# Kernel optimization log

Hardware: AMD Instinct MI355X
Metric: run time of the kernel (lower is better)

The kernel has to match this reference:

```python
import jax, jax.numpy as jnp
import numpy as np

EPS = 1e-5

def _bn(h):
    # BatchNorm1d, affine=False, track_running_stats=False -> batch stats, biased var
    m = h.mean(axis=0)
    v = h.var(axis=0)
    return (h - m) * jax.lax.rsqrt(v + EPS)

def _aggregate(x, edge_index):
    # out[i] = sum over edges (i <- j) of x[j]  + x[i] (self loop)
    dst, src = edge_index[0], edge_index[1]
    n = x.shape[0]
    return jax.ops.segment_sum(x[src], dst, num_segments=n) + x

def setup_inputs() -> dict:
    key = jax.random.key(0)
    ks = jax.random.split(key, 12)
    N, F, H, C, E = 100000, 128, 128, 40, 800000
    x = jax.random.normal(ks[0], (N, F), dtype=jnp.float32)
    edge_index = jax.random.randint(ks[1], (2, E), 0, N, dtype=jnp.int64)
    def lin(kw, kb, fan_in, fan_out):
        bound = 1.0 / np.sqrt(fan_in)
        W = jax.random.uniform(kw, (fan_in, fan_out), minval=-bound, maxval=bound, dtype=jnp.float32)
        b = jax.random.uniform(kb, (fan_out,), minval=-bound, maxval=bound, dtype=jnp.float32)
        return W, b
    W0, b0 = lin(ks[2], ks[3], F, H)
    W1, b1 = lin(ks[4], ks[5], H, H)
    W2, b2 = lin(ks[6], ks[7], H, H)
    Wl, bl = lin(ks[8], ks[9], H, C)
    return {"x": x, "edge_index": edge_index, "W0": W0, "b0": b0,
            "W1": W1, "b1": b1, "W2": W2, "b2": b2, "Wl": Wl, "bl": bl}

def reference(x, edge_index, W0, b0, W1, b1, W2, b2, Wl, bl):
    h = x
    for W, b in ((W0, b0), (W1, b1), (W2, b2)):
        h = _aggregate(h, edge_index)          # spmm(A + I, h)
        h = h @ W + b                          # Linear
        h = _bn(h)                             # BatchNorm1d (no affine)
        h = jax.nn.relu(h)
    return h @ Wl + bl
```

## Files before the change

### kernel.cpp

```cpp
#include <hip/hip_runtime.h>
#include <stdint.h>

typedef __attribute__((ext_vector_type(8))) short short8;
typedef __attribute__((ext_vector_type(4))) float floatx4;

static __device__ __forceinline__ float b2f(uint16_t b){
    return __uint_as_float(((uint32_t)b) << 16);
}
static __device__ __forceinline__ uint16_t f2b(float f){
    uint32_t u = __float_as_uint(f);
    return (uint16_t)((u + 0x7fffu + ((u >> 16) & 1u)) >> 16);
}
static __device__ __forceinline__ float blo(uint32_t v){ return __uint_as_float(v << 16); }
static __device__ __forceinline__ float bhi(uint32_t v){ return __uint_as_float(v & 0xffff0000u); }
static __device__ __forceinline__ uint32_t pack2(float a, float b){
    return ((uint32_t)f2b(b) << 16) | (uint32_t)f2b(a);
}

__global__ void k_sentinel(uint32_t* out, int nwords, uint32_t pat){
    int i = blockIdx.x * blockDim.x + threadIdx.x;
    if (i < nwords) out[i] = pat;
}

__global__ void k_zf(int* deg, int N, const uint32_t* xw, const int* ei, int* flags,
                     float* stats, int ZB){
    if ((int)blockIdx.x == ZB){
        if (threadIdx.x != 0) return;
        int odd_nz = 0;
        for (int k = 0; k < 128; k++){
            if (ei[2 * k + 1] != 0) odd_nz = 1;
        }
        flags[0] = odd_nz ? 0 : 1;
        int big = 0;
        for (int k = 0; k < 128; k++){
            float lo = __uint_as_float(xw[k] << 16);
            if (!(fabsf(lo) <= 1024.0f)) big = 1;
        }
        flags[1] = big ? 0 : 1;
        return;
    }
    if ((int)blockIdx.x == ZB + 1){
        int t = threadIdx.x;
        #pragma unroll
        for (int j = 0; j < 3; j++) stats[j * 256 + t] = 0.f;
        return;
    }
    int i = blockIdx.x * blockDim.x + threadIdx.x;
    if (i < N) deg[i] = 0;
}

__global__ void k_deg(const int* ei, int E, int* deg, uint16_t* rank, const int* flags){
    int e = blockIdx.x * blockDim.x + threadIdx.x;
    if (e < E){
        int d = flags[0] ? ei[2 * e] : ei[e];
        int r = atomicAdd(&deg[d], 1);
        rank[e] = (uint16_t)r;
    }
}

__global__ void k_scan1(const int* deg, int N, int* bsum){
    __shared__ int s[256];
    int t = threadIdx.x;
    int i = blockIdx.x * 256 + t;
    s[t] = (i < N) ? deg[i] : 0;
    __syncthreads();
    for (int off = 128; off > 0; off >>= 1){
        if (t < off) s[t] += s[t + off];
        __syncthreads();
    }
    if (t == 0) bsum[blockIdx.x] = s[0];
}

__global__ void k_scan2(int* bsum, int nb, int* rp, int N){
    __shared__ int s[512];
    int t = threadIdx.x;
    int v = (t < nb) ? bsum[t] : 0;
    s[t] = v;
    __syncthreads();
    for (int off = 1; off < 512; off <<= 1){
        int u = (t >= off) ? s[t - off] : 0;
        __syncthreads();
        s[t] += u;
        __syncthreads();
    }
    if (t < nb) bsum[t] = s[t] - v;
    if (t == 511) rp[N] = s[511];
}

__global__ void k_scan3(const int* deg, int N, const int* bpre, int* rp){
    __shared__ int s[256];
    int t = threadIdx.x;
    int i = blockIdx.x * 256 + t;
    int v = (i < N) ? deg[i] : 0;
    s[t] = v;
    __syncthreads();
    for (int off = 1; off < 256; off <<= 1){
        int u = (t >= off) ? s[t - off] : 0;
        __syncthreads();
        s[t] += u;
        __syncthreads();
    }
    if (i < N) rp[i] = bpre[blockIdx.x] + s[t] - v;
}

__global__ __launch_bounds__(256) void k_fill(const int* __restrict__ ei, int E,
                                              const int* __restrict__ rp,
                                              const uint16_t* __restrict__ rank,
                                              int* __restrict__ col,
                                              const int* __restrict__ flags, int N){
    int xcd = blockIdx.x & 7;
    int sub = blockIdx.x >> 3;
    int nsub = gridDim.x >> 3;
    int r0 = (int)(((long long)N * xcd) >> 3);
    int r1 = (int)(((long long)N * (xcd + 1)) >> 3);
    int e0 = (int)(((long long)E * sub) / nsub);
    int e1 = (int)(((long long)E * (sub + 1)) / nsub);
    int is64 = flags[0];
    for (int e = e0 + threadIdx.x; e < e1; e += 256){
        int d = is64 ? ei[2 * e] : ei[e];
        if (d >= r0 && d < r1){
            int sv = is64 ? ei[2 * (E + e)] : ei[E + e];
            int p = rp[d] + (int)rank[e];
            col[p] = sv;
        }
    }
}

__global__ void k_prep(const void* W0, const void* W1, const void* W2, const void* Wl,
                       uint16_t* Wf0, uint16_t* Wf1, uint16_t* Wf2, uint16_t* Wfl,
                       const void* b0, const void* b1, const void* b2, const void* bl,
                       float* bc, const void* x, uint16_t* hx, int NF,
                       const int* flags){
    int blk = blockIdx.x;
    int t = threadIdx.x;
    if (blk >= 218){
        if (flags[1]) return;
        int nb = gridDim.x - 218;
        int n8 = NF >> 3;
        const float4* xv = (const float4*)x;
        uint4* hv = (uint4*)hx;
        for (int i = (blk - 218) * 256 + t; i < n8; i += nb * 256){
            float4 u0 = xv[i * 2];
            float4 u1 = xv[i * 2 + 1];
            uint4 o;
            o.x = pack2(u0.x, u0.y); o.y = pack2(u0.z, u0.w);
            o.z = pack2(u1.x, u1.y); o.w = pack2(u1.z, u1.w);
            hv[i] = o;
        }
        return;
    }
    if (blk >= 216){
        int i = (blk - 216) * 256 + t;
        if (i >= 424) return;
        const void* src; int li;
        if (i < 128)      { src = b0; li = i; }
        else if (i < 256) { src = b1; li = i - 128; }
        else if (i < 384) { src = b2; li = i - 256; }
        else              { src = bl; li = i - 384; }
        bc[i] = flags[1] ? b2f(((const uint16_t*)src)[li]) : ((const float*)src)[li];
        return;
    }
    const void* W; uint16_t* Wf; int C, ntiles, lb;
    if (blk < 64)        { W = W0; Wf = Wf0; C = 128; ntiles = 8; lb = blk; }
    else if (blk < 128)  { W = W1; Wf = Wf1; C = 128; ntiles = 8; lb = blk - 64; }
    else if (blk < 192)  { W = W2; Wf = Wf2; C = 128; ntiles = 8; lb = blk - 128; }
    else                 { W = Wl; Wf = Wfl; C = 40;  ntiles = 3; lb = blk - 192; }
    int idx = lb * 256 + t;
    int total = 4 * ntiles * 512;
    if (idx >= total) return;
    int j = idx & 7;
    int lane = (idx >> 3) & 63;
    int nt = (idx >> 9) % ntiles;
    int kt = idx / (512 * ntiles);
    int k = kt * 32 + (lane >> 4) * 8 + j;
    int n = nt * 16 + (lane & 15);
    uint16_t v = 0;
    if (n < C){
        v = flags[1] ? ((const uint16_t*)W)[k * C + n]
                     : f2b(((const float*)W)[k * C + n]);
    }
    Wf[idx] = v;
}

__global__ __launch_bounds__(256) void k_ag(const uint16_t* __restrict__ Yin,
                                            const uint16_t* __restrict__ xraw,
                                            const int* __restrict__ rp,
                                            const int* __restrict__ col,
                                            uint16_t* __restrict__ Yout,
                                            const uint16_t* __restrict__ Wf,
                                            const float* __restrict__ bias,
                                            float* __restrict__ part, int N,
                                            const float* __restrict__ st,
                                            int apply_bn, float ninv,
                                            const int* __restrict__ flags){
    __shared__ __align__(16) uint16_t albs[2048];
    __shared__ float sh_sum[128], sh_ssq[128];
    int t = threadIdx.x;
    if (t < 128){ sh_sum[t] = 0.f; sh_ssq[t] = 0.f; }
    int l16 = t & 15;
    int r = t >> 4;
    int row = blockIdx.x * 16 + r;
    int i = (row < N) ? row : N - 1;
    float tt[8], iv[8];
    const uint16_t* src = Yin;
    if (apply_bn){
        int f0 = l16 * 8;
        #pragma unroll
        for (int j = 0; j < 8; j++){
            float sv = st[f0 + j];
            float qv = st[128 + f0 + j];
            float m = sv * ninv;
            float var = qv * ninv - m * m;
            float ivj = rsqrtf(var + 1e-5f);
            iv[j] = ivj;
            tt[j] = -m * ivj;
        }
    } else if (flags[1]){
        src = xraw;
    }
    const uint4* base = (const uint4*)src;
    int s0 = rp[i], e0 = rp[i + 1];
    float a[8];
    {
        uint4 w = base[(size_t)i * 16 + l16];
        a[0] = blo(w.x); a[1] = bhi(w.x); a[2] = blo(w.y); a[3] = bhi(w.y);
        a[4] = blo(w.z); a[5] = bhi(w.z); a[6] = blo(w.w); a[7] = bhi(w.w);
        if (apply_bn){
            #pragma unroll
            for (int jj = 0; jj < 8; jj++) a[jj] = fmaxf(fmaf(a[jj], iv[jj], tt[jj]), 0.f);
        }
    }
    int k = s0;
    for (; k + 3 < e0; k += 4){
        int j0 = col[k], j1 = col[k + 1], j2 = col[k + 2], j3 = col[k + 3];
        uint4 ww[4];
        ww[0] = base[(size_t)j0 * 16 + l16];
        ww[1] = base[(size_t)j1 * 16 + l16];
        ww[2] = base[(size_t)j2 * 16 + l16];
        ww[3] = base[(size_t)j3 * 16 + l16];
        #pragma unroll
        for (int u = 0; u < 4; u++){
            float v[8] = {blo(ww[u].x), bhi(ww[u].x), blo(ww[u].y), bhi(ww[u].y),
                          blo(ww[u].z), bhi(ww[u].z), blo(ww[u].w), bhi(ww[u].w)};
            if (apply_bn){
                #pragma unroll
                for (int jj = 0; jj < 8; jj++) v[jj] = fmaxf(fmaf(v[jj], iv[jj], tt[jj]), 0.f);
            }
            #pragma unroll
            for (int jj = 0; jj < 8; jj++) a[jj] += v[jj];
        }
    }
    for (; k < e0; k++){
        int j = col[k];
        uint4 w = base[(size_t)j * 16 + l16];
        float v[8] = {blo(w.x), bhi(w.x), blo(w.y), bhi(w.y),
                      blo(w.z), bhi(w.z), blo(w.w), bhi(w.w)};
        if (apply_bn){
            #pragma unroll
            for (int jj = 0; jj < 8; jj++) v[jj] = fmaxf(fmaf(v[jj], iv[jj], tt[jj]), 0.f);
        }
        #pragma unroll
        for (int jj = 0; jj < 8; jj++) a[jj] += v[jj];
    }
    {
        uint4 o;
        o.x = pack2(a[0], a[1]); o.y = pack2(a[2], a[3]);
        o.z = pack2(a[4], a[5]); o.w = pack2(a[6], a[7]);
        int wb = r * 256 + ((l16 * 16) ^ ((r & 7) << 4));
        *(uint4*)((char*)albs + wb) = o;
    }
    __syncthreads();
    int lane = t & 63, wave = t >> 6;
    int m = lane & 15, q = lane >> 4;
    short8 af[4];
    #pragma unroll
    for (int kt = 0; kt < 4; kt++){
        int rb = m * 256 + ((kt * 64 + q * 16) ^ ((m & 7) << 4));
        af[kt] = *(const short8*)((const char*)albs + rb);
    }
    const short8* wg = (const short8*)Wf;
    floatx4 acc[2];
    acc[0] = (floatx4){0.f, 0.f, 0.f, 0.f};
    acc[1] = (floatx4){0.f, 0.f, 0.f, 0.f};
    #pragma unroll
    for (int kt = 0; kt < 4; kt++){
        #pragma unroll
        for (int n2 = 0; n2 < 2; n2++){
            short8 bf = wg[(kt * 8 + wave * 2 + n2) * 64 + lane];
            acc[n2] = __builtin_amdgcn_mfma_f32_16x16x32_bf16(af[kt], bf, acc[n2], 0, 0, 0);
        }
    }
    int row_base = blockIdx.x * 16;
    #pragma unroll
    for (int n2 = 0; n2 < 2; n2++){
        int ccol = (wave * 2 + n2) * 16 + m;
        float bv = bias[ccol];
        float s = 0.f, ss = 0.f;
        #pragma unroll
        for (int rr = 0; rr < 4; rr++){
            int grow = row_base + q * 4 + rr;
            if (grow < N){
                float y = acc[n2][rr] + bv;
                Yout[(size_t)grow * 128 + ccol] = f2b(y);
                s += y;
                ss += y * y;
            }
        }
        s += __shfl_xor(s, 16); s += __shfl_xor(s, 32);
        ss += __shfl_xor(ss, 16); ss += __shfl_xor(ss, 32);
        if (q == 0){
            atomicAdd(&sh_sum[ccol], s);
            atomicAdd(&sh_ssq[ccol], ss);
        }
    }
    __syncthreads();
    if (t < 128){
        part[(size_t)blockIdx.x * 256 + t] = sh_sum[t];
        part[(size_t)blockIdx.x * 256 + 128 + t] = sh_ssq[t];
    }
}

__global__ __launch_bounds__(256) void k_red(const float* __restrict__ part, int nb,
                                             float* __restrict__ st){
    int t = threadIdx.x;
    int r0 = blockIdx.x * 32;
    int r1 = r0 + 32; if (r1 > nb) r1 = nb;
    float s0 = 0.f, s1 = 0.f, s2 = 0.f, s3 = 0.f;
    int b = r0;
    for (; b + 3 < r1; b += 4){
        s0 += part[(size_t)b * 256 + t];
        s1 += part[(size_t)(b + 1) * 256 + t];
        s2 += part[(size_t)(b + 2) * 256 + t];
        s3 += part[(size_t)(b + 3) * 256 + t];
    }
    for (; b < r1; b++) s0 += part[(size_t)b * 256 + t];
    atomicAdd(&st[t], (s0 + s1) + (s2 + s3));
}

__global__ __launch_bounds__(256) void k_out(const uint16_t* __restrict__ A,
                                             const uint16_t* __restrict__ Wf,
                                             const float* __restrict__ bias,
                                             const float* __restrict__ st, float ninv,
                                             void* __restrict__ out, int N,
                                             const int* __restrict__ flags){
    __shared__ __align__(16) uint16_t wlds[6144];
    __shared__ float s_m[128], s_iv[128];
    int t = threadIdx.x;
    {
        const uint4* s = (const uint4*)Wf;
        uint4* d = (uint4*)wlds;
        for (int i = t; i < 768; i += 256) d[i] = s[i];
    }
    if (t < 128){
        float m = st[t] * ninv;
        float var = st[128 + t] * ninv - m * m;
        s_m[t] = m;
        s_iv[t] = rsqrtf(var + 1e-5f);
    }
    __syncthreads();
    int lane = t & 63, wave = t >> 6;
    int m = lane & 15, q = lane >> 4;
    int row_base = blockIdx.x * 64 + wave * 16;
    int arow = row_base + m;
    if (arow >= N) arow = N - 1;
    short8 afrag[4];
    const uint4* ap = (const uint4*)(A + (size_t)arow * 128);
    #pragma unroll
    for (int kt = 0; kt < 4; kt++){
        uint4 u = ap[kt * 4 + q];
        float v[8] = {blo(u.x), bhi(u.x), blo(u.y), bhi(u.y),
                      blo(u.z), bhi(u.z), blo(u.w), bhi(u.w)};
        int c0 = kt * 32 + q * 8;
        #pragma unroll
        for (int j = 0; j < 8; j++) v[j] = fmaxf((v[j] - s_m[c0 + j]) * s_iv[c0 + j], 0.f);
        uint4 o;
        o.x = pack2(v[0], v[1]); o.y = pack2(v[2], v[3]);
        o.z = pack2(v[4], v[5]); o.w = pack2(v[6], v[7]);
        afrag[kt] = *(short8*)&o;
    }
    floatx4 acc[3];
    #pragma unroll
    for (int nt = 0; nt < 3; nt++) acc[nt] = (floatx4){0.f, 0.f, 0.f, 0.f};
    const short8* wl = (const short8*)wlds;
    #pragma unroll
    for (int kt = 0; kt < 4; kt++){
        #pragma unroll
        for (int nt = 0; nt < 3; nt++){
            acc[nt] = __builtin_amdgcn_mfma_f32_16x16x32_bf16(afrag[kt], wl[(kt * 3 + nt) * 64 + lane], acc[nt], 0, 0, 0);
        }
    }
    int isbf = flags[1];
    #pragma unroll
    for (int nt = 0; nt < 3; nt++){
        int ccol = nt * 16 + m;
        if (ccol < 40){
            float bv = bias[ccol];
            #pragma unroll
            for (int r = 0; r < 4; r++){
                int grow = row_base + q * 4 + r;
                if (grow < N){
                    float y = acc[nt][r] + bv;
                    if (isbf) ((uint16_t*)out)[(size_t)grow * 40 + ccol] = f2b(y);
                    else      ((float*)out)[(size_t)grow * 40 + ccol] = y;
                }
            }
        }
    }
}

extern "C" void kernel_launch(void* const* d_in, const int* in_sizes, int n_in,
                              void* d_out, int out_size, void* d_ws, size_t ws_size,
                              hipStream_t stream){
    (void)n_in;
    const void* x  = d_in[0];
    const int* ei  = (const int*)d_in[1];
    const void* W0 = d_in[2];
    const void* b0 = d_in[3];
    const void* W1 = d_in[4];
    const void* b1 = d_in[5];
    const void* W2 = d_in[6];
    const void* b2 = d_in[7];
    const void* Wl = d_in[8];
    const void* bl = d_in[9];

    const int N = in_sizes[0] / 128;
    const int E = in_sizes[1] / 2;
    const int NF = N * 128;
    const int NB = (N + 255) / 256;
    const int agg_blocks  = (N + 15) / 16;
    const int gemm_blocks = (N + 63) / 64;
    const int red_blocks  = (agg_blocks + 31) / 32;

    char* ws = (char*)d_ws;
    size_t off = 0;
    uint16_t* hx = (uint16_t*)(ws + off); off += ((size_t)NF * 2 + 255) & ~(size_t)255;
    uint16_t* ag = (uint16_t*)(ws + off); off += ((size_t)NF * 2 + 255) & ~(size_t)255;
    int* col     = (int*)(ws + off);      off += ((size_t)E * 4 + 255) & ~(size_t)255;
    int* rp      = (int*)(ws + off);      off += ((size_t)(N + 1) * 4 + 255) & ~(size_t)255;
    uint16_t* rank = (uint16_t*)(ws + off); off += ((size_t)E * 2 + 255) & ~(size_t)255;
    int* deg     = (int*)(ws + off);      off += ((size_t)N * 4 + 255) & ~(size_t)255;
    int* bsum    = (int*)(ws + off);      off += 512 * 4;
    int* flags   = (int*)(ws + off);      off += 256;
    uint16_t* Wf0 = (uint16_t*)(ws + off); off += 16384 * 2;
    uint16_t* Wf1 = (uint16_t*)(ws + off); off += 16384 * 2;
    uint16_t* Wf2 = (uint16_t*)(ws + off); off += 16384 * 2;
    uint16_t* Wfl = (uint16_t*)(ws + off); off += 6144 * 2;
    float* bc    = (float*)(ws + off);    off += 424 * 4 + 160;
    float* stats = (float*)(ws + off);    off += 768 * 4;
    float* part  = (float*)(ws + off);    off += (size_t)agg_blocks * 256 * 4;
    const size_t required = off;

    if (ws_size < required){
        int nwords = out_size / 2;
        k_sentinel<<<(nwords + 255) / 256, 256, 0, stream>>>((uint32_t*)d_out, nwords, 0x40004000u);
        return;
    }

    k_zf<<<NB + 2, 256, 0, stream>>>(deg, N, (const uint32_t*)x, ei, flags, stats, NB);
    k_deg<<<(E + 255) / 256, 256, 0, stream>>>(ei, E, deg, rank, flags);
    k_scan1<<<NB, 256, 0, stream>>>(deg, N, bsum);
    k_scan2<<<1, 512, 0, stream>>>(bsum, NB, rp, N);
    k_scan3<<<NB, 256, 0, stream>>>(deg, N, bsum, rp);
    k_fill<<<1024, 256, 0, stream>>>(ei, E, rp, rank, col, flags, N);

    k_prep<<<2266, 256, 0, stream>>>(W0, W1, W2, Wl, Wf0, Wf1, Wf2, Wfl,
                                     b0, b1, b2, bl, bc, x, hx, NF, flags);

    const float ninv = 1.0f / (float)N;
    const uint16_t* xr = (const uint16_t*)x;

    k_ag<<<agg_blocks, 256, 0, stream>>>(hx, xr, rp, col, ag, Wf0, bc, part, N,
                                         stats, 0, ninv, flags);
    k_red<<<red_blocks, 256, 0, stream>>>(part, agg_blocks, stats);
    k_ag<<<agg_blocks, 256, 0, stream>>>(ag, xr, rp, col, hx, Wf1, bc + 128, part, N,
                                         stats, 1, ninv, flags);
    k_red<<<red_blocks, 256, 0, stream>>>(part, agg_blocks, stats + 256);
    k_ag<<<agg_blocks, 256, 0, stream>>>(hx, xr, rp, col, ag, Wf2, bc + 256, part, N,
                                         stats + 256, 1, ninv, flags);
    k_red<<<red_blocks, 256, 0, stream>>>(part, agg_blocks, stats + 512);
    k_out<<<gemm_blocks, 256, 0, stream>>>(ag, Wfl, bc + 384, stats + 512, ninv, d_out, N, flags);
}
```

Before: 373.7 us.

## Make each wave own a 16-row tile to drop block barriers in aggregate-GEMM

Restructures the fused aggregate+linear kernel so that each wave gathers 16 rows on its own (4 rows per pass, 4 passes), writes them to a private LDS slice and computes all 8 output column tiles with MFMA. The block-wide __syncthreads and the shared-memory atomic reduction of the BN statistics are removed, and per-wave partials go straight to global memory, which gives four times as many partial rows for k_red. The aim is to remove barrier stalls and load imbalance between waves with different row degrees. In exchange each wave holds more accumulators and runs a serial gather loop over its 4 row groups, and more Wf loads are issued per wave.

```diff
diff --git a/kernel.cpp b/kernel.cpp
--- a/kernel.cpp
+++ b/kernel.cpp
@@ -193,18 +193,17 @@
                                             const float* __restrict__ st,
                                             int apply_bn, float ninv,
                                             const int* __restrict__ flags){
-    __shared__ __align__(16) uint16_t albs[2048];
-    __shared__ float sh_sum[128], sh_ssq[128];
-    int t = threadIdx.x;
-    if (t < 128){ sh_sum[t] = 0.f; sh_ssq[t] = 0.f; }
-    int l16 = t & 15;
-    int r = t >> 4;
-    int row = blockIdx.x * 16 + r;
-    int i = (row < N) ? row : N - 1;
+    __shared__ __align__(16) uint16_t albs[8192];
+    int t = threadIdx.x;
+    int lane = t & 63, wave = t >> 6;
+    int tile = blockIdx.x * 4 + wave;
+    int row_base = tile * 16;
+    int c = lane & 15;
+    int rg = lane >> 4;
     float tt[8], iv[8];
     const uint16_t* src = Yin;
     if (apply_bn){
-        int f0 = l16 * 8;
+        int f0 = c * 8;
         #pragma unroll
         for (int j = 0; j < 8; j++){
             float sv = st[f0 + j];
@@ -219,29 +218,48 @@
         src = xraw;
     }
     const uint4* base = (const uint4*)src;
-    int s0 = rp[i], e0 = rp[i + 1];
-    float a[8];
-    {
-        uint4 w = base[(size_t)i * 16 + l16];
-        a[0] = blo(w.x); a[1] = bhi(w.x); a[2] = blo(w.y); a[3] = bhi(w.y);
-        a[4] = blo(w.z); a[5] = bhi(w.z); a[6] = blo(w.w); a[7] = bhi(w.w);
-        if (apply_bn){
+    char* my = (char*)albs + wave * 4096;
+    #pragma unroll
+    for (int g = 0; g < 4; g++){
+        int r = g * 4 + rg;
+        int row = row_base + r;
+        int i = (row < N) ? row : N - 1;
+        int s0 = rp[i], e0 = rp[i + 1];
+        float a[8];
+        {
+            uint4 w = base[(size_t)i * 16 + c];
+            a[0] = blo(w.x); a[1] = bhi(w.x); a[2] = blo(w.y); a[3] = bhi(w.y);
+            a[4] = blo(w.z); a[5] = bhi(w.z); a[6] = blo(w.w); a[7] = bhi(w.w);
+            if (apply_bn){
+                #pragma unroll
+                for (int jj = 0; jj < 8; jj++) a[jj] = fmaxf(fmaf(a[jj], iv[jj], tt[jj]), 0.f);
+            }
+        }
+        int k = s0;
+        for (; k + 3 < e0; k += 4){
+            int j0 = col[k], j1 = col[k + 1], j2 = col[k + 2], j3 = col[k + 3];
+            uint4 ww[4];
+            ww[0] = base[(size_t)j0 * 16 + c];
+            ww[1] = base[(size_t)j1 * 16 + c];
+            ww[2] = base[(size_t)j2 * 16 + c];
+            ww[3] = base[(size_t)j3 * 16 + c];
             #pragma unroll
-            for (int jj = 0; jj < 8; jj++) a[jj] = fmaxf(fmaf(a[jj], iv[jj], tt[jj]), 0.f);
-        }
-    }
-    int k = s0;
-    for (; k + 3 < e0; k += 4){
-        int j0 = col[k], j1 = col[k + 1], j2 = col[k + 2], j3 = col[k + 3];
-        uint4 ww[4];
-        ww[0] = base[(size_t)j0 * 16 + l16];
-        ww[1] = base[(size_t)j1 * 16 + l16];
-        ww[2] = base[(size_t)j2 * 16 + l16];
-        ww[3] = base[(size_t)j3 * 16 + l16];
-        #pragma unroll
-        for (int u = 0; u < 4; u++){
-            float v[8] = {blo(ww[u].x), bhi(ww[u].x), blo(ww[u].y), bhi(ww[u].y),
-                          blo(ww[u].z), bhi(ww[u].z), blo(ww[u].w), bhi(ww[u].w)};
+            for (int u = 0; u < 4; u++){
+                float v[8] = {blo(ww[u].x), bhi(ww[u].x), blo(ww[u].y), bhi(ww[u].y),
+                              blo(ww[u].z), bhi(ww[u].z), blo(ww[u].w), bhi(ww[u].w)};
+                if (apply_bn){
+                    #pragma unroll
+                    for (int jj = 0; jj < 8; jj++) v[jj] = fmaxf(fmaf(v[jj], iv[jj], tt[jj]), 0.f);
+                }
+                #pragma unroll
+                for (int jj = 0; jj < 8; jj++) a[jj] += v[jj];
+            }
+        }
+        for (; k < e0; k++){
+            int j = col[k];
+            uint4 w = base[(size_t)j * 16 + c];
+            float v[8] = {blo(w.x), bhi(w.x), blo(w.y), bhi(w.y),
+                          blo(w.z), bhi(w.z), blo(w.w), bhi(w.w)};
             if (apply_bn){
                 #pragma unroll
                 for (int jj = 0; jj < 8; jj++) v[jj] = fmaxf(fmaf(v[jj], iv[jj], tt[jj]), 0.f);
@@ -249,58 +267,43 @@
             #pragma unroll
             for (int jj = 0; jj < 8; jj++) a[jj] += v[jj];
         }
-    }
-    for (; k < e0; k++){
-        int j = col[k];
-        uint4 w = base[(size_t)j * 16 + l16];
-        float v[8] = {blo(w.x), bhi(w.x), blo(w.y), bhi(w.y),
-                      blo(w.z), bhi(w.z), blo(w.w), bhi(w.w)};
-        if (apply_bn){
-            #pragma unroll
-            for (int jj = 0; jj < 8; jj++) v[jj] = fmaxf(fmaf(v[jj], iv[jj], tt[jj]), 0.f);
-        }
-        #pragma unroll
-        for (int jj = 0; jj < 8; jj++) a[jj] += v[jj];
-    }
-    {
-        uint4 o;
-        o.x = pack2(a[0], a[1]); o.y = pack2(a[2], a[3]);
-        o.z = pack2(a[4], a[5]); o.w = pack2(a[6], a[7]);
-        int wb = r * 256 + ((l16 * 16) ^ ((r & 7) << 4));
-        *(uint4*)((char*)albs + wb) = o;
-    }
-    __syncthreads();
-    int lane = t & 63, wave = t >> 6;
+        {
+            uint4 o;
+            o.x = pack2(a[0], a[1]); o.y = pack2(a[2], a[3]);
+            o.z = pack2(a[4], a[5]); o.w = pack2(a[6], a[7]);
+            int wb = r * 256 + ((c * 16) ^ ((r & 7) << 4));
+            *(uint4*)(my + wb) = o;
+        }
+    }
     int m = lane & 15, q = lane >> 4;
     short8 af[4];
     #pragma unroll
     for (int kt = 0; kt < 4; kt++){
         int rb = m * 256 + ((kt * 64 + q * 16) ^ ((m & 7) << 4));
-        af[kt] = *(const short8*)((const char*)albs + rb);
+        af[kt] = *(const short8*)(my + rb);
     }
     const short8* wg = (const short8*)Wf;
-    floatx4 acc[2];
-    acc[0] = (floatx4){0.f, 0.f, 0.f, 0.f};
-    acc[1] = (floatx4){0.f, 0.f, 0.f, 0.f};
+    floatx4 acc[8];
+    #pragma unroll
+    for (int nt = 0; nt < 8; nt++) acc[nt] = (floatx4){0.f, 0.f, 0.f, 0.f};
     #pragma unroll
     for (int kt = 0; kt < 4; kt++){
         #pragma unroll
-        for (int n2 = 0; n2 < 2; n2++){
-            short8 bf = wg[(kt * 8 + wave * 2 + n2) * 64 + lane];
-            acc[n2] = __builtin_amdgcn_mfma_f32_16x16x32_bf16(af[kt], bf, acc[n2], 0, 0, 0);
-        }
-    }
-    int row_base = blockIdx.x * 16;
-    #pragma unroll
-    for (int n2 = 0; n2 < 2; n2++){
-        int ccol = (wave * 2 + n2) * 16 + m;
+        for (int nt = 0; nt < 8; nt++){
+            short8 bf = wg[(kt * 8 + nt) * 64 + lane];
+            acc[nt] = __builtin_amdgcn_mfma_f32_16x16x32_bf16(af[kt], bf, acc[nt], 0, 0, 0);
+        }
+    }
+    #pragma unroll
+    for (int nt = 0; nt < 8; nt++){
+        int ccol = nt * 16 + m;
         float bv = bias[ccol];
         float s = 0.f, ss = 0.f;
         #pragma unroll
         for (int rr = 0; rr < 4; rr++){
             int grow = row_base + q * 4 + rr;
             if (grow < N){
-                float y = acc[n2][rr] + bv;
+                float y = acc[nt][rr] + bv;
                 Yout[(size_t)grow * 128 + ccol] = f2b(y);
                 s += y;
                 ss += y * y;
@@ -309,14 +312,9 @@
         s += __shfl_xor(s, 16); s += __shfl_xor(s, 32);
         ss += __shfl_xor(ss, 16); ss += __shfl_xor(ss, 32);
         if (q == 0){
-            atomicAdd(&sh_sum[ccol], s);
-            atomicAdd(&sh_ssq[ccol], ss);
-        }
-    }
-    __syncthreads();
-    if (t < 128){
-        part[(size_t)blockIdx.x * 256 + t] = sh_sum[t];
-        part[(size_t)blockIdx.x * 256 + 128 + t] = sh_ssq[t];
+            part[(size_t)tile * 256 + ccol] = s;
+            part[(size_t)tile * 256 + 128 + ccol] = ss;
+        }
     }
 }
 
@@ -427,9 +425,10 @@
     const int E = in_sizes[1] / 2;
     const int NF = N * 128;
     const int NB = (N + 255) / 256;
-    const int agg_blocks  = (N + 15) / 16;
+    const int agg_grid   = (N + 63) / 64;
+    const int agg_tiles  = agg_grid * 4;
     const int gemm_blocks = (N + 63) / 64;
-    const int red_blocks  = (agg_blocks + 31) / 32;
+    const int red_blocks  = (agg_tiles + 31) / 32;
 
     char* ws = (char*)d_ws;
     size_t off = 0;
@@ -447,7 +446,7 @@
     uint16_t* Wfl = (uint16_t*)(ws + off); off += 6144 * 2;
     float* bc    = (float*)(ws + off);    off += 424 * 4 + 160;
     float* stats = (float*)(ws + off);    off += 768 * 4;
-    float* part  = (float*)(ws + off);    off += (size_t)agg_blocks * 256 * 4;
+    float* part  = (float*)(ws + off);    off += (size_t)agg_tiles * 256 * 4;
     const size_t required = off;
 
     if (ws_size < required){
@@ -469,14 +468,14 @@
     const float ninv = 1.0f / (float)N;
     const uint16_t* xr = (const uint16_t*)x;
 
-    k_ag<<<agg_blocks, 256, 0, stream>>>(hx, xr, rp, col, ag, Wf0, bc, part, N,
-                                         stats, 0, ninv, flags);
-    k_red<<<red_blocks, 256, 0, stream>>>(part, agg_blocks, stats);
-    k_ag<<<agg_blocks, 256, 0, stream>>>(ag, xr, rp, col, hx, Wf1, bc + 128, part, N,
-                                         stats, 1, ninv, flags);
-    k_red<<<red_blocks, 256, 0, stream>>>(part, agg_blocks, stats + 256);
-    k_ag<<<agg_blocks, 256, 0, stream>>>(hx, xr, rp, col, ag, Wf2, bc + 256, part, N,
-                                         stats + 256, 1, ninv, flags);
-    k_red<<<red_blocks, 256, 0, stream>>>(part, agg_blocks, stats + 512);
+    k_ag<<<agg_grid, 256, 0, stream>>>(hx, xr, rp, col, ag, Wf0, bc, part, N,
+                                       stats, 0, ninv, flags);
+    k_red<<<red_blocks, 256, 0, stream>>>(part, agg_tiles, stats);
+    k_ag<<<agg_grid, 256, 0, stream>>>(ag, xr, rp, col, hx, Wf1, bc + 128, part, N,
+                                       stats, 1, ninv, flags);
+    k_red<<<red_blocks, 256, 0, stream>>>(part, agg_tiles, stats + 256);
+    k_ag<<<agg_grid, 256, 0, stream>>>(hx, xr, rp, col, ag, Wf2, bc + 256, part, N,
+                                       stats + 256, 1, ninv, flags);
+    k_red<<<red_blocks, 256, 0, stream>>>(part, agg_tiles, stats + 512);
     k_out<<<gemm_blocks, 256, 0, stream>>>(ag, Wfl, bc + 384, stats + 512, ninv, d_out, N, flags);
 }
```

Result: slower. 400.6 us (+7.2%).

## Split fused aggregate+GEMM into separate gather and LDS-tiled GEMM kernels

Applied to the files above, without the earlier changes.

Unfuses the per-layer kernel into a pure sparse aggregation kernel that writes bf16 rows to global memory and a separate GEMM kernel. The GEMM stages the whole weight matrix in LDS and processes 128 rows per block with an in-place bias add, store and BN partial-stat reduction. The aim is to remove the per-16-row weight reload from global memory and the syncthreads/LDS staging from the latency-bound gather kernel. The cost is an extra round trip of the aggregated activation through HBM (read and write of N×128 bf16) and one extra launch per layer.

```diff
diff --git a/kernel.cpp b/kernel.cpp
--- a/kernel.cpp
+++ b/kernel.cpp
@@ -182,25 +182,18 @@
     Wf[idx] = v;
 }
 
-__global__ __launch_bounds__(256) void k_ag(const uint16_t* __restrict__ Yin,
-                                            const uint16_t* __restrict__ xraw,
-                                            const int* __restrict__ rp,
-                                            const int* __restrict__ col,
-                                            uint16_t* __restrict__ Yout,
-                                            const uint16_t* __restrict__ Wf,
-                                            const float* __restrict__ bias,
-                                            float* __restrict__ part, int N,
-                                            const float* __restrict__ st,
-                                            int apply_bn, float ninv,
-                                            const int* __restrict__ flags){
-    __shared__ __align__(16) uint16_t albs[2048];
-    __shared__ float sh_sum[128], sh_ssq[128];
-    int t = threadIdx.x;
-    if (t < 128){ sh_sum[t] = 0.f; sh_ssq[t] = 0.f; }
+__global__ __launch_bounds__(256) void k_agg(const uint16_t* __restrict__ Yin,
+                                             const uint16_t* __restrict__ xraw,
+                                             const int* __restrict__ rp,
+                                             const int* __restrict__ col,
+                                             uint16_t* __restrict__ out, int N,
+                                             const float* __restrict__ st,
+                                             int apply_bn, float ninv,
+                                             const int* __restrict__ flags){
+    int t = threadIdx.x;
     int l16 = t & 15;
-    int r = t >> 4;
-    int row = blockIdx.x * 16 + r;
-    int i = (row < N) ? row : N - 1;
+    int i = blockIdx.x * 16 + (t >> 4);
+    if (i >= N) return;
     float tt[8], iv[8];
     const uint16_t* src = Yin;
     if (apply_bn){
@@ -262,55 +255,80 @@
         #pragma unroll
         for (int jj = 0; jj < 8; jj++) a[jj] += v[jj];
     }
+    uint4 o;
+    o.x = pack2(a[0], a[1]); o.y = pack2(a[2], a[3]);
+    o.z = pack2(a[4], a[5]); o.w = pack2(a[6], a[7]);
+    ((uint4*)out)[(size_t)i * 16 + l16] = o;
+}
+
+__global__ __launch_bounds__(256) void k_gemm(uint16_t* __restrict__ A,
+                                              const uint16_t* __restrict__ Wf,
+                                              const float* __restrict__ bias,
+                                              float* __restrict__ part, int N){
+    __shared__ __align__(16) uint16_t wlds[16384];
+    __shared__ float sh_sum[128], sh_ssq[128];
+    int t = threadIdx.x;
+    if (t < 128){ sh_sum[t] = 0.f; sh_ssq[t] = 0.f; }
     {
-        uint4 o;
-        o.x = pack2(a[0], a[1]); o.y = pack2(a[2], a[3]);
-        o.z = pack2(a[4], a[5]); o.w = pack2(a[6], a[7]);
-        int wb = r * 256 + ((l16 * 16) ^ ((r & 7) << 4));
-        *(uint4*)((char*)albs + wb) = o;
+        const uint4* s = (const uint4*)Wf;
+        uint4* d = (uint4*)wlds;
+        for (int i = t; i < 2048; i += 256) d[i] = s[i];
     }
     __syncthreads();
     int lane = t & 63, wave = t >> 6;
     int m = lane & 15, q = lane >> 4;
-    short8 af[4];
+    int rb[2];
+    rb[0] = blockIdx.x * 128 + wave * 16;
+    rb[1] = rb[0] + 64;
+    short8 afrag[2][4];
+    #pragma unroll
+    for (int mt = 0; mt < 2; mt++){
+        int arow = rb[mt] + m;
+        if (arow >= N) arow = N - 1;
+        const short8* ap = (const short8*)(A + (size_t)arow * 128);
+        #pragma unroll
+        for (int kt = 0; kt < 4; kt++) afrag[mt][kt] = ap[kt * 4 + q];
+    }
+    floatx4 acc[2][8];
+    #pragma unroll
+    for (int mt = 0; mt < 2; mt++)
+        #pragma unroll
+        for (int nt = 0; nt < 8; nt++) acc[mt][nt] = (floatx4){0.f, 0.f, 0.f, 0.f};
+    const short8* wl = (const short8*)wlds;
     #pragma unroll
     for (int kt = 0; kt < 4; kt++){
-        int rb = m * 256 + ((kt * 64 + q * 16) ^ ((m & 7) << 4));
-        af[kt] = *(const short8*)((const char*)albs + rb);
-    }
-    const short8* wg = (const short8*)Wf;
-    floatx4 acc[2];
-    acc[0] = (floatx4){0.f, 0.f, 0.f, 0.f};
-    acc[1] = (floatx4){0.f, 0.f, 0.f, 0.f};
-    #pragma unroll
-    for (int kt = 0; kt < 4; kt++){
-        #pragma unroll
-        for (int n2 = 0; n2 < 2; n2++){
-            short8 bf = wg[(kt * 8 + wave * 2 + n2) * 64 + lane];
-            acc[n2] = __builtin_amdgcn_mfma_f32_16x16x32_bf16(af[kt], bf, acc[n2], 0, 0, 0);
-        }
-    }
-    int row_base = blockIdx.x * 16;
-    #pragma unroll
-    for (int n2 = 0; n2 < 2; n2++){
-        int ccol = (wave * 2 + n2) * 16 + m;
-        float bv = bias[ccol];
-        float s = 0.f, ss = 0.f;
-        #pragma unroll
-        for (int rr = 0; rr < 4; rr++){
-            int grow = row_base + q * 4 + rr;
-            if (grow < N){
-                float y = acc[n2][rr] + bv;
-                Yout[(size_t)grow * 128 + ccol] = f2b(y);
-                s += y;
-                ss += y * y;
+        #pragma unroll
+        for (int nt = 0; nt < 8; nt++){
+            short8 bfrag = wl[(kt * 8 + nt) * 64 + lane];
+            #pragma unroll
+            for (int mt = 0; mt < 2; mt++){
+                acc[mt][nt] = __builtin_amdgcn_mfma_f32_16x16x32_bf16(afrag[mt][kt], bfrag, acc[mt][nt], 0, 0, 0);
             }
         }
-        s += __shfl_xor(s, 16); s += __shfl_xor(s, 32);
-        ss += __shfl_xor(ss, 16); ss += __shfl_xor(ss, 32);
-        if (q == 0){
-            atomicAdd(&sh_sum[ccol], s);
-            atomicAdd(&sh_ssq[ccol], ss);
+    }
+    #pragma unroll
+    for (int mt = 0; mt < 2; mt++){
+        #pragma unroll
+        for (int nt = 0; nt < 8; nt++){
+            int ccol = nt * 16 + m;
+            float bv = bias[ccol];
+            float s = 0.f, ss = 0.f;
+            #pragma unroll
+            for (int r = 0; r < 4; r++){
+                int grow = rb[mt] + q * 4 + r;
+                if (grow < N){
+                    float y = acc[mt][nt][r] + bv;
+                    A[(size_t)grow * 128 + ccol] = f2b(y);
+                    s += y;
+                    ss += y * y;
+                }
+            }
+            s += __shfl_xor(s, 16); s += __shfl_xor(s, 32);
+            ss += __shfl_xor(ss, 16); ss += __shfl_xor(ss, 32);
+            if (q == 0){
+                atomicAdd(&sh_sum[ccol], s);
+                atomicAdd(&sh_ssq[ccol], ss);
+            }
         }
     }
     __syncthreads();
@@ -427,9 +445,10 @@
     const int E = in_sizes[1] / 2;
     const int NF = N * 128;
     const int NB = (N + 255) / 256;
-    const int agg_blocks  = (N + 15) / 16;
-    const int gemm_blocks = (N + 63) / 64;
-    const int red_blocks  = (agg_blocks + 31) / 32;
+    const int agg_blocks   = (N + 15) / 16;
+    const int gemm_blocks2 = (N + 127) / 128;
+    const int gemm_blocks  = (N + 63) / 64;
+    const int red_blocks   = (gemm_blocks2 + 31) / 32;
 
     char* ws = (char*)d_ws;
     size_t off = 0;
@@ -447,7 +466,7 @@
     uint16_t* Wfl = (uint16_t*)(ws + off); off += 6144 * 2;
     float* bc    = (float*)(ws + off);    off += 424 * 4 + 160;
     float* stats = (float*)(ws + off);    off += 768 * 4;
-    float* part  = (float*)(ws + off);    off += (size_t)agg_blocks * 256 * 4;
+    float* part  = (float*)(ws + off);    off += (size_t)gemm_blocks2 * 256 * 4;
     const size_t required = off;
 
     if (ws_size < required){
@@ -469,14 +488,14 @@
     const float ninv = 1.0f / (float)N;
     const uint16_t* xr = (const uint16_t*)x;
 
-    k_ag<<<agg_blocks, 256, 0, stream>>>(hx, xr, rp, col, ag, Wf0, bc, part, N,
-                                         stats, 0, ninv, flags);
-    k_red<<<red_blocks, 256, 0, stream>>>(part, agg_blocks, stats);
-    k_ag<<<agg_blocks, 256, 0, stream>>>(ag, xr, rp, col, hx, Wf1, bc + 128, part, N,
-                                         stats, 1, ninv, flags);
-    k_red<<<red_blocks, 256, 0, stream>>>(part, agg_blocks, stats + 256);
-    k_ag<<<agg_blocks, 256, 0, stream>>>(hx, xr, rp, col, ag, Wf2, bc + 256, part, N,
-                                         stats + 256, 1, ninv, flags);
-    k_red<<<red_blocks, 256, 0, stream>>>(part, agg_blocks, stats + 512);
+    k_agg<<<agg_blocks, 256, 0, stream>>>(hx, xr, rp, col, ag, N, stats, 0, ninv, flags);
+    k_gemm<<<gemm_blocks2, 256, 0, stream>>>(ag, Wf0, bc, part, N);
+    k_red<<<red_blocks, 256, 0, stream>>>(part, gemm_blocks2, stats);
+    k_agg<<<agg_blocks, 256, 0, stream>>>(ag, xr, rp, col, hx, N, stats, 1, ninv, flags);
+    k_gemm<<<gemm_blocks2, 256, 0, stream>>>(hx, Wf1, bc + 128, part, N);
+    k_red<<<red_blocks, 256, 0, stream>>>(part, gemm_blocks2, stats + 256);
+    k_agg<<<agg_blocks, 256, 0, stream>>>(hx, xr, rp, col, ag, N, stats + 256, 1, ninv, flags);
+    k_gemm<<<gemm_blocks2, 256, 0, stream>>>(ag, Wf2, bc + 256, part, N);
+    k_red<<<red_blocks, 256, 0, stream>>>(part, gemm_blocks2, stats + 512);
     k_out<<<gemm_blocks, 256, 0, stream>>>(ag, Wfl, bc + 384, stats + 512, ninv, d_out, N, flags);
 }
```

New measurement: 384.9 us. 3.0% more time.
